# Kernel tuning notes

Measured on AMD Instinct MI355X. Metric: run time of the kernel, lower is better.

Reference implementation:

```python
import jax, jax.numpy as jnp
import numpy as np

TWO_PI = 2.0 * np.pi

def setup_inputs() -> dict:
    key = jax.random.key(0)
    k1, k2, k3 = jax.random.split(key, 3)
    S, B, T = 272, 128, 1024          # sensors, batch, time
    J, H = 128, 32                    # output channels, harmonics
    X = jax.random.normal(k1, (S, B, T), dtype=jnp.float32)
    sensor_locs = jax.random.uniform(k2, (S, 2), dtype=jnp.float32)
    fourier_weights = jax.random.normal(k3, (J, H, H, 2), dtype=jnp.float32)
    return {"X": X, "sensor_locs": sensor_locs, "fourier_weights": fourier_weights}


def reference(X, sensor_locs, fourier_weights):
    # Normalize sensor locations to [0, 1] per coordinate (as in torch code).
    lo = sensor_locs.min(axis=0)
    hi = sensor_locs.max(axis=0)
    locs = (sensor_locs - lo) / (hi - lo)                      # [S, 2]

    H = fourier_weights.shape[1]
    harm = jnp.arange(H, dtype=locs.dtype)
    # phase[s, k, l] = 2*pi*(k * x_s + l * y_s)
    phase = TWO_PI * (locs[:, 0, None, None] * harm[None, :, None]
                      + locs[:, 1, None, None] * harm[None, None, :])  # [S, H, H]

    # Separable Fourier-feature contraction replacing the triple Python loop:
    # attn_maps[s, j] = sum_{k,l} Wr[j,k,l]*cos(phase[s,k,l]) + Wi[j,k,l]*sin(phase[s,k,l])
    attn_maps = (jnp.einsum('skl,jkl->sj', jnp.cos(phase), fourier_weights[..., 0])
                 + jnp.einsum('skl,jkl->sj', jnp.sin(phase), fourier_weights[..., 1]))  # [S, J]

    attention_weights = jax.nn.softmax(attn_maps, axis=-1)     # softmax over output channels

    # torch.einsum('bi,bjk->bjk', attn, X): sum attn over i, scale X elementwise.
    return jnp.einsum('si,sjk->sjk', attention_weights, X)
```

## Files before the change

kernel.cpp:

```cpp
#include <hip/hip_runtime.h>
#include <hip/hip_bf16.h>


#define NS 272
#define NJ 128
#define KL 1024
#define BT_LOG2_F4 15
#define N4 8912896

__global__ __launch_bounds__(256) void scale_kernel(
    const float* __restrict__ locs,
    const float* __restrict__ W,
    float* __restrict__ scale)
{
    __shared__ float cosv[2][KL];
    __shared__ float sinv[2][KL];
    __shared__ float mm[4][4];
    __shared__ float wred[4];

    const int tid  = threadIdx.x;
    const int lane = tid & 63;
    const int wave = tid >> 6;
    const int sensLocal = tid >> 7;
    const int s = blockIdx.x * 2 + sensLocal;
    const int jt = tid & 127;

    float lx = 1e30f, ly = 1e30f, hx = -1e30f, hy = -1e30f;
    for (int i = tid; i < NS; i += 256) {
        float x = locs[2 * i], y = locs[2 * i + 1];
        lx = fminf(lx, x); hx = fmaxf(hx, x);
        ly = fminf(ly, y); hy = fmaxf(hy, y);
    }
#pragma unroll
    for (int off = 32; off; off >>= 1) {
        lx = fminf(lx, __shfl_xor(lx, off));
        hx = fmaxf(hx, __shfl_xor(hx, off));
        ly = fminf(ly, __shfl_xor(ly, off));
        hy = fmaxf(hy, __shfl_xor(hy, off));
    }
    if (lane == 0) { mm[wave][0] = lx; mm[wave][1] = hx; mm[wave][2] = ly; mm[wave][3] = hy; }
    __syncthreads();
    lx = fminf(fminf(mm[0][0], mm[1][0]), fminf(mm[2][0], mm[3][0]));
    hx = fmaxf(fmaxf(mm[0][1], mm[1][1]), fmaxf(mm[2][1], mm[3][1]));
    ly = fminf(fminf(mm[0][2], mm[1][2]), fminf(mm[2][2], mm[3][2]));
    hy = fmaxf(fmaxf(mm[0][3], mm[1][3]), fmaxf(mm[2][3], mm[3][3]));

    const float xs = (locs[2 * s]     - lx) / (hx - lx);
    const float ys = (locs[2 * s + 1] - ly) / (hy - ly);

    const float TWO_PI = 6.283185307179586f;
    for (int idx = jt; idx < KL; idx += 128) {
        int k = idx >> 5, l = idx & 31;
        float ph = TWO_PI * (xs * (float)k + ys * (float)l);
        float c, sn;
        sincosf(ph, &sn, &c);
        cosv[sensLocal][idx] = c;
        sinv[sensLocal][idx] = sn;
    }
    __syncthreads();

    const float4* W4 = (const float4*)(W + (size_t)jt * 2048);
    const float* cv = cosv[sensLocal];
    const float* sv = sinv[sensLocal];
    float acc = 0.0f;
#pragma unroll 4
    for (int kl = 0; kl < KL; kl += 2) {
        float4 w = W4[kl >> 1];
        acc = fmaf(w.x, cv[kl],     acc);
        acc = fmaf(w.y, sv[kl],     acc);
        acc = fmaf(w.z, cv[kl + 1], acc);
        acc = fmaf(w.w, sv[kl + 1], acc);
    }

    float m = acc;
#pragma unroll
    for (int off = 32; off; off >>= 1) m = fmaxf(m, __shfl_xor(m, off));
    if (lane == 0) wred[wave] = m;
    __syncthreads();
    m = fmaxf(wred[sensLocal * 2], wred[sensLocal * 2 + 1]);
    __syncthreads();

    float e = expf(acc - m);
    float t = e;
#pragma unroll
    for (int off = 32; off; off >>= 1) t += __shfl_xor(t, off);
    if (lane == 0) wred[wave] = t;
    __syncthreads();
    float denom = wred[sensLocal * 2] + wred[sensLocal * 2 + 1];
    __syncthreads();

    float part = e / denom;
    t = part;
#pragma unroll
    for (int off = 32; off; off >>= 1) t += __shfl_xor(t, off);
    if (lane == 0) wred[wave] = t;
    __syncthreads();
    if (jt == 0) scale[s] = wred[sensLocal * 2] + wred[sensLocal * 2 + 1];
}

__global__ __launch_bounds__(256) void scale_x_kernel(
    const float4* __restrict__ X,
    const float* __restrict__ scale,
    float4* __restrict__ out)
{
    int i = blockIdx.x * 256 + threadIdx.x;
    const int stride = gridDim.x * 256;
    for (; i < N4; i += stride) {
        float sc = scale[i >> BT_LOG2_F4];
        float4 v = X[i];
        v.x *= sc; v.y *= sc; v.z *= sc; v.w *= sc;
        out[i] = v;
    }
}

extern "C" void kernel_launch(void* const* d_in, const int* in_sizes, int n_in,
                              void* d_out, int out_size, void* d_ws, size_t ws_size,
                              hipStream_t stream) {
    const float* X    = (const float*)d_in[0];
    const float* locs = (const float*)d_in[1];
    const float* W    = (const float*)d_in[2];
    float* out   = (float*)d_out;
    float* scale = (float*)d_ws;

    scale_kernel<<<NS / 2, 256, 0, stream>>>(locs, W, scale);
    scale_x_kernel<<<2048, 256, 0, stream>>>((const float4*)X, scale, (float4*)out);
}
```

Measured before the change: 321.8 us.

## Restructure scale kernel per-sensor and use nontemporal stores in scaling kernel

The scale kernel now handles one sensor per block, with pairs of threads splitting each output channel's dot product. It stores cos/sin values interleaved as float4 so they line up with the weight layout, and uses separate reduction buffers to drop extra barriers. The X-scaling kernel now gives each block a fixed 16-iteration chunk of a single sensor, so the scale is loaded once per block. Results are written with nontemporal stores to cut cache pollution on the large streaming output. This launches more blocks for the small kernel and relies on the exact problem sizes being hardcoded.

```diff
diff --git a/kernel.cpp b/kernel.cpp
--- a/kernel.cpp
+++ b/kernel.cpp
@@ -5,25 +5,22 @@
 #define NS 272
 #define NJ 128
 #define KL 1024
-#define BT_LOG2_F4 15
-#define N4 8912896
+
+typedef float v4f __attribute__((ext_vector_type(4)));
 
 __global__ __launch_bounds__(256) void scale_kernel(
     const float* __restrict__ locs,
     const float* __restrict__ W,
     float* __restrict__ scale)
 {
-    __shared__ float cosv[2][KL];
-    __shared__ float sinv[2][KL];
+    __shared__ float4 trig[KL / 2];
     __shared__ float mm[4][4];
-    __shared__ float wred[4];
+    __shared__ float wredA[4], wredB[4], wredC[4];
 
     const int tid  = threadIdx.x;
     const int lane = tid & 63;
     const int wave = tid >> 6;
-    const int sensLocal = tid >> 7;
-    const int s = blockIdx.x * 2 + sensLocal;
-    const int jt = tid & 127;
+    const int s = blockIdx.x;
 
     float lx = 1e30f, ly = 1e30f, hx = -1e30f, hy = -1e30f;
     for (int i = tid; i < NS; i += 256) {
@@ -49,67 +46,74 @@
     const float ys = (locs[2 * s + 1] - ly) / (hy - ly);
 
     const float TWO_PI = 6.283185307179586f;
-    for (int idx = jt; idx < KL; idx += 128) {
-        int k = idx >> 5, l = idx & 31;
-        float ph = TWO_PI * (xs * (float)k + ys * (float)l);
-        float c, sn;
-        sincosf(ph, &sn, &c);
-        cosv[sensLocal][idx] = c;
-        sinv[sensLocal][idx] = sn;
+#pragma unroll
+    for (int m = tid; m < KL / 2; m += 256) {
+        int kl0 = 2 * m, kl1 = 2 * m + 1;
+        float ph0 = TWO_PI * (xs * (float)(kl0 >> 5) + ys * (float)(kl0 & 31));
+        float ph1 = TWO_PI * (xs * (float)(kl1 >> 5) + ys * (float)(kl1 & 31));
+        float c0, s0, c1, s1;
+        sincosf(ph0, &s0, &c0);
+        sincosf(ph1, &s1, &c1);
+        trig[m] = make_float4(c0, s0, c1, s1);
     }
     __syncthreads();
 
-    const float4* W4 = (const float4*)(W + (size_t)jt * 2048);
-    const float* cv = cosv[sensLocal];
-    const float* sv = sinv[sensLocal];
-    float acc = 0.0f;
-#pragma unroll 4
-    for (int kl = 0; kl < KL; kl += 2) {
-        float4 w = W4[kl >> 1];
-        acc = fmaf(w.x, cv[kl],     acc);
-        acc = fmaf(w.y, sv[kl],     acc);
-        acc = fmaf(w.z, cv[kl + 1], acc);
-        acc = fmaf(w.w, sv[kl + 1], acc);
+    const int j    = tid >> 1;
+    const int half = tid & 1;
+    const float4* __restrict__ W4 = (const float4*)W + (size_t)j * 512 + half * 256;
+    const float4* __restrict__ T4 = trig + half * 256;
+    float a0 = 0.f, a1 = 0.f, a2 = 0.f, a3 = 0.f;
+#pragma unroll 8
+    for (int i = 0; i < 256; ++i) {
+        float4 w = W4[i];
+        float4 t = T4[i];
+        a0 = fmaf(w.x, t.x, a0);
+        a1 = fmaf(w.y, t.y, a1);
+        a2 = fmaf(w.z, t.z, a2);
+        a3 = fmaf(w.w, t.w, a3);
     }
+    float acc = (a0 + a1) + (a2 + a3);
+    acc += __shfl_xor(acc, 1);
 
     float m = acc;
 #pragma unroll
     for (int off = 32; off; off >>= 1) m = fmaxf(m, __shfl_xor(m, off));
-    if (lane == 0) wred[wave] = m;
+    if (lane == 0) wredA[wave] = m;
     __syncthreads();
-    m = fmaxf(wred[sensLocal * 2], wred[sensLocal * 2 + 1]);
-    __syncthreads();
+    m = fmaxf(fmaxf(wredA[0], wredA[1]), fmaxf(wredA[2], wredA[3]));
 
     float e = expf(acc - m);
     float t = e;
 #pragma unroll
     for (int off = 32; off; off >>= 1) t += __shfl_xor(t, off);
-    if (lane == 0) wred[wave] = t;
+    if (lane == 0) wredB[wave] = t;
     __syncthreads();
-    float denom = wred[sensLocal * 2] + wred[sensLocal * 2 + 1];
-    __syncthreads();
+    float denom = 0.5f * ((wredB[0] + wredB[1]) + (wredB[2] + wredB[3]));
 
     float part = e / denom;
     t = part;
 #pragma unroll
     for (int off = 32; off; off >>= 1) t += __shfl_xor(t, off);
-    if (lane == 0) wred[wave] = t;
+    if (lane == 0) wredC[wave] = t;
     __syncthreads();
-    if (jt == 0) scale[s] = wred[sensLocal * 2] + wred[sensLocal * 2 + 1];
+    if (tid == 0)
+        scale[s] = 0.5f * ((wredC[0] + wredC[1]) + (wredC[2] + wredC[3]));
 }
 
 __global__ __launch_bounds__(256) void scale_x_kernel(
-    const float4* __restrict__ X,
+    const v4f* __restrict__ X,
     const float* __restrict__ scale,
-    float4* __restrict__ out)
+    v4f* __restrict__ out)
 {
-    int i = blockIdx.x * 256 + threadIdx.x;
-    const int stride = gridDim.x * 256;
-    for (; i < N4; i += stride) {
-        float sc = scale[i >> BT_LOG2_F4];
-        float4 v = X[i];
-        v.x *= sc; v.y *= sc; v.z *= sc; v.w *= sc;
-        out[i] = v;
+    const int bid = blockIdx.x;
+    const int s = bid >> 3;
+    const float sc = scale[s];
+    const int base = (s << 15) + ((bid & 7) << 12) + threadIdx.x;
+#pragma unroll
+    for (int it = 0; it < 16; ++it) {
+        int i = base + (it << 8);
+        v4f v = X[i] * sc;
+        __builtin_nontemporal_store(v, &out[i]);
     }
 }
 
@@ -122,6 +126,6 @@
     float* out   = (float*)d_out;
     float* scale = (float*)d_ws;
 
-    scale_kernel<<<NS / 2, 256, 0, stream>>>(locs, W, scale);
-    scale_x_kernel<<<2048, 256, 0, stream>>>((const float4*)X, scale, (float4*)out);
+    scale_kernel<<<NS, 256, 0, stream>>>(locs, W, scale);
+    scale_x_kernel<<<NS * 8, 256, 0, stream>>>((const v4f*)X, scale, (v4f*)out);
 }
```

Result: no change. 317.0 us (-1.5%).
